# Kernel tuning notes

Hardware: AMD Instinct MI355X
Metric: run time of the kernel (lower is better)

The kernel has to match this reference:

```python
import jax, jax.numpy as jnp
import numpy as np

IN_FEATURES = 8192
OUT_FEATURES = 8192
LOG2_IN = 13
LOG2_OUT = 13
Q_LEVELS = 2 ** 4 - 1  # 15, 4-bit quantization levels


def _rot_mats(angles):
    # (m,) angles -> (m, 2, 2) Givens rotation matrices (QuIP gen_rand_orthos p=2 fast path)
    c, s = jnp.cos(angles), jnp.sin(angles)
    return jnp.stack([jnp.stack([c, s], axis=-1), jnp.stack([-s, c], axis=-1)], axis=-2)


def _mul_ortho_butterfly(angles, p_in, p_out, x):
    # QuIP mul_ortho_butterfly for n = 2^L: input permutation, L stages of
    # block-diagonal 2x2 rotations each followed by a stride-interleave, output permutation.
    n, q = x.shape
    x = x[p_in]
    for i in range(angles.shape[0]):  # static stage count (log2 n)
        B = _rot_mats(angles[i])                             # (n/2, 2, 2)
        x = jnp.einsum('mij,mjq->miq', B, x.reshape(n // 2, 2, q))
        x = jnp.transpose(x, (1, 0, 2)).reshape(n, q)        # interleave stride permutation
    return x[p_out]


def setup_inputs() -> dict:
    key = jax.random.key(0)
    ks = jax.random.split(key, 12)
    x = jax.random.normal(ks[0], (1, IN_FEATURES), dtype=jnp.float32)
    qweight = jax.random.randint(ks[1], (IN_FEATURES, OUT_FEATURES), 0, 16, dtype=jnp.int32)
    # +0.5 keeps the per-feature divisor away from zero (it divides x)
    scaleWH = jax.random.uniform(ks[2], (IN_FEATURES,), dtype=jnp.float32) + 0.5
    scale = jax.random.uniform(ks[3], (), dtype=jnp.float32) + 0.5
    bias = jax.random.normal(ks[4], (OUT_FEATURES,), dtype=jnp.float32)
    two_pi = 2.0 * np.float32(np.pi)
    U_angles = jax.random.uniform(ks[5], (LOG2_OUT, OUT_FEATURES // 2), dtype=jnp.float32) * two_pi
    V_angles = jax.random.uniform(ks[6], (LOG2_IN, IN_FEATURES // 2), dtype=jnp.float32) * two_pi
    pU_in = jax.random.permutation(ks[7], OUT_FEATURES).astype(jnp.int32)
    pU_out = jax.random.permutation(ks[8], OUT_FEATURES).astype(jnp.int32)
    pV_in = jax.random.permutation(ks[9], IN_FEATURES).astype(jnp.int32)
    pV_out = jax.random.permutation(ks[10], IN_FEATURES).astype(jnp.int32)
    return {"x": x, "qweight": qweight, "scaleWH": scaleWH, "scale": scale, "bias": bias,
            "U_angles": U_angles, "V_angles": V_angles,
            "pU_in": pU_in, "pU_out": pU_out, "pV_in": pV_in, "pV_out": pV_out}


def reference(x, qweight, scaleWH, scale, bias, U_angles, V_angles, pU_in, pU_out, pV_in, pV_out):
    # dequantize: w in [0, 15] -> [-1, 1], then global scale
    w = qweight.T.astype(jnp.float32)                 # (out, in)
    w_fast = (w / Q_LEVELS * 2.0 - 1.0) * scale
    h = (x / scaleWH).T                               # (in, 1) reverse diag scaling
    h = _mul_ortho_butterfly(V_angles, pV_in, pV_out, h)   # V^T-side incoherence transform
    h = w_fast @ h                                    # (out, 1) single-token GEMV
    h = _mul_ortho_butterfly(U_angles, pU_in, pU_out, h).T  # (1, out) U-side transform
    return h + bias
```

## Files before the change

### kernel.cpp

```cpp
#include <hip/hip_runtime.h>

#define IN_F   8192
#define OUT_F  8192
#define HALF_F 4096
#define STAGES 13

#define KCHUNK 64
#define NCHUNK (IN_F / KCHUNK)
#define OTILE  1024

typedef int   v4i __attribute__((ext_vector_type(4)));
typedef float v4f __attribute__((ext_vector_type(4)));

__global__ __launch_bounds__(1024) void butterfly_in_kernel(
    const float* __restrict__ x, const float* __restrict__ scaleWH,
    const float* __restrict__ V_angles, const int* __restrict__ pin,
    const int* __restrict__ pout, float* __restrict__ h_out,
    float* __restrict__ sum_out)
{
    __shared__ float bufA[IN_F];
    __shared__ float bufB[IN_F];
    const int tid = threadIdx.x;

#pragma unroll
    for (int j = 0; j < 8; ++j) {
        int k = tid + j * 1024;
        int src = pin[k];
        bufA[k] = x[src] / scaleWH[src];
    }
    __syncthreads();

    float* in = bufA;
    float* out = bufB;
    for (int s = 0; s < STAGES; ++s) {
        const float* ang = V_angles + s * HALF_F;
#pragma unroll
        for (int j = 0; j < 4; ++j) {
            int m = tid + j * 1024;
            float c, sn;
            __sincosf(ang[m], &sn, &c);
            float x0 = in[2 * m];
            float x1 = in[2 * m + 1];
            out[m]          =  c * x0 + sn * x1;
            out[HALF_F + m] = -sn * x0 + c * x1;
        }
        __syncthreads();
        float* t = in; in = out; out = t;
    }

    float local = 0.0f;
#pragma unroll
    for (int j = 0; j < 8; ++j) {
        int k = tid + j * 1024;
        float v = in[pout[k]];
        h_out[k] = v;
        local += v;
    }
    __syncthreads();
    float* red = out;
    red[tid] = local;
    __syncthreads();
    for (int s = 512; s > 0; s >>= 1) {
        if (tid < s) red[tid] += red[tid + s];
        __syncthreads();
    }
    if (tid == 0) *sum_out = red[0];
}

__global__ __launch_bounds__(256) void gemv_kernel(
    const int* __restrict__ q, const float* __restrict__ h,
    float* __restrict__ partials)
{
    __shared__ float hs[KCHUNK];
    const int tid = threadIdx.x;
    const int ot = blockIdx.x;
    const int kc = blockIdx.y;
    const int i0 = kc * KCHUNK;

    if (tid < KCHUNK) hs[tid] = h[i0 + tid];
    __syncthreads();

    const int o = ot * OTILE + tid * 4;
    const int* qp = q + (size_t)i0 * OUT_F + o;

    float a0 = 0.f, a1 = 0.f, a2 = 0.f, a3 = 0.f;
#pragma unroll 4
    for (int ii = 0; ii < KCHUNK; ++ii) {
        v4i v = __builtin_nontemporal_load((const v4i*)qp);
        qp += OUT_F;
        float hv = hs[ii];
        a0 += hv * (float)v[0];
        a1 += hv * (float)v[1];
        a2 += hv * (float)v[2];
        a3 += hv * (float)v[3];
    }
    v4f r; r[0] = a0; r[1] = a1; r[2] = a2; r[3] = a3;
    *(v4f*)(partials + (size_t)kc * OUT_F + o) = r;
}

__global__ __launch_bounds__(256) void reduce_kernel(
    const float* __restrict__ partials, float* __restrict__ accum)
{
    const int o = blockIdx.x * 256 + threadIdx.x;
    float s = 0.0f;
#pragma unroll 8
    for (int c = 0; c < NCHUNK; ++c) s += partials[(size_t)c * OUT_F + o];
    accum[o] = s;
}

__global__ __launch_bounds__(1024) void butterfly_out_kernel(
    const float* __restrict__ accum, const float* __restrict__ sum_h_p,
    const float* __restrict__ scale_p, const float* __restrict__ bias,
    const float* __restrict__ U_angles, const int* __restrict__ pin,
    const int* __restrict__ pout, float* __restrict__ out_f)
{
    __shared__ float bufA[OUT_F];
    __shared__ float bufB[OUT_F];
    const int tid = threadIdx.x;
    const float scale = *scale_p;
    const float sum_h = *sum_h_p;

#pragma unroll
    for (int j = 0; j < 8; ++j) {
        int k = tid + j * 1024;
        bufA[k] = scale * ((2.0f / 15.0f) * accum[k] - sum_h);
    }
    __syncthreads();
#pragma unroll
    for (int j = 0; j < 8; ++j) {
        int k = tid + j * 1024;
        bufB[k] = bufA[pin[k]];
    }
    __syncthreads();

    float* in = bufB;
    float* out = bufA;
    for (int s = 0; s < STAGES; ++s) {
        const float* ang = U_angles + s * HALF_F;
#pragma unroll
        for (int j = 0; j < 4; ++j) {
            int m = tid + j * 1024;
            float c, sn;
            __sincosf(ang[m], &sn, &c);
            float x0 = in[2 * m];
            float x1 = in[2 * m + 1];
            out[m]          =  c * x0 + sn * x1;
            out[HALF_F + m] = -sn * x0 + c * x1;
        }
        __syncthreads();
        float* t = in; in = out; out = t;
    }

#pragma unroll
    for (int j = 0; j < 8; ++j) {
        int k = tid + j * 1024;
        out_f[k] = in[pout[k]] + bias[k];
    }
}

extern "C" void kernel_launch(void* const* d_in, const int* in_sizes, int n_in,
                              void* d_out, int out_size, void* d_ws, size_t ws_size,
                              hipStream_t stream) {
    const float* x        = (const float*)d_in[0];
    const int*   qweight  = (const int*)  d_in[1];
    const float* scaleWH  = (const float*)d_in[2];
    const float* scale    = (const float*)d_in[3];
    const float* bias     = (const float*)d_in[4];
    const float* U_angles = (const float*)d_in[5];
    const float* V_angles = (const float*)d_in[6];
    const int*   pU_in    = (const int*)  d_in[7];
    const int*   pU_out   = (const int*)  d_in[8];
    const int*   pV_in    = (const int*)  d_in[9];
    const int*   pV_out   = (const int*)  d_in[10];
    float* out = (float*)d_out;

    float* h        = (float*)d_ws;
    float* sum_h    = h + IN_F;
    float* accum    = sum_h + 8;
    float* partials = accum + OUT_F;

    butterfly_in_kernel<<<1, 1024, 0, stream>>>(
        x, scaleWH, V_angles, pV_in, pV_out, h, sum_h);

    gemv_kernel<<<dim3(OUT_F / OTILE, NCHUNK), 256, 0, stream>>>(
        qweight, h, partials);

    reduce_kernel<<<OUT_F / 256, 256, 0, stream>>>(partials, accum);

    butterfly_out_kernel<<<1, 1024, 0, stream>>>(
        accum, sum_h, scale, bias, U_angles, pU_in, pU_out, out);
}
```

Baseline: 396.2 us.

## Prefetch weight head into cache during input butterfly, fuse dequant into reduce

While the single-block input butterfly runs, 96 extra blocks read the first part of the quantized weight matrix so it is resident in L2/MALL before the GEMV starts, overlapping weight streaming with the serial butterfly. The dequant affine step moves from the output butterfly into the reduce kernel, which removes one shared-memory pass and a sync. KCHUNK doubles, halving the number of partial sums the reduce must read. The prefetch adds extra memory traffic, and the cached data may be evicted or compete with the butterfly block.

```diff
diff --git a/kernel.cpp b/kernel.cpp
--- a/kernel.cpp
+++ b/kernel.cpp
@@ -5,9 +5,12 @@
 #define HALF_F 4096
 #define STAGES 13
 
-#define KCHUNK 64
+#define KCHUNK 128
 #define NCHUNK (IN_F / KCHUNK)
 #define OTILE  1024
+
+#define PF_BLOCKS 96
+#define PF_ITERS  16
 
 typedef int   v4i __attribute__((ext_vector_type(4)));
 typedef float v4f __attribute__((ext_vector_type(4)));
@@ -16,11 +19,26 @@
     const float* __restrict__ x, const float* __restrict__ scaleWH,
     const float* __restrict__ V_angles, const int* __restrict__ pin,
     const int* __restrict__ pout, float* __restrict__ h_out,
-    float* __restrict__ sum_out)
-{
+    float* __restrict__ sum_out, const int* __restrict__ q,
+    int* __restrict__ scratch)
+{
+    const int tid = threadIdx.x;
+
+    if (blockIdx.x != 0) {
+        const int pf = blockIdx.x - 1;
+        const int* base = q + (size_t)pf * (1024 * PF_ITERS * 4);
+        int acc = 0;
+#pragma unroll
+        for (int it = 0; it < PF_ITERS; ++it) {
+            v4i v = *(const v4i*)(base + (it * 1024 + tid) * 4);
+            acc ^= v[0] ^ v[1] ^ v[2] ^ v[3];
+        }
+        if (tid == 0) scratch[pf] = acc;
+        return;
+    }
+
     __shared__ float bufA[IN_F];
     __shared__ float bufB[IN_F];
-    const int tid = threadIdx.x;
 
 #pragma unroll
     for (int j = 0; j < 8; ++j) {
@@ -99,37 +117,29 @@
 }
 
 __global__ __launch_bounds__(256) void reduce_kernel(
-    const float* __restrict__ partials, float* __restrict__ accum)
+    const float* __restrict__ partials, const float* __restrict__ sum_h_p,
+    const float* __restrict__ scale_p, float* __restrict__ t_out)
 {
     const int o = blockIdx.x * 256 + threadIdx.x;
     float s = 0.0f;
 #pragma unroll 8
     for (int c = 0; c < NCHUNK; ++c) s += partials[(size_t)c * OUT_F + o];
-    accum[o] = s;
+    t_out[o] = (*scale_p) * ((2.0f / 15.0f) * s - (*sum_h_p));
 }
 
 __global__ __launch_bounds__(1024) void butterfly_out_kernel(
-    const float* __restrict__ accum, const float* __restrict__ sum_h_p,
-    const float* __restrict__ scale_p, const float* __restrict__ bias,
+    const float* __restrict__ t, const float* __restrict__ bias,
     const float* __restrict__ U_angles, const int* __restrict__ pin,
     const int* __restrict__ pout, float* __restrict__ out_f)
 {
     __shared__ float bufA[OUT_F];
     __shared__ float bufB[OUT_F];
     const int tid = threadIdx.x;
-    const float scale = *scale_p;
-    const float sum_h = *sum_h_p;
-
-#pragma unroll
-    for (int j = 0; j < 8; ++j) {
-        int k = tid + j * 1024;
-        bufA[k] = scale * ((2.0f / 15.0f) * accum[k] - sum_h);
-    }
-    __syncthreads();
-#pragma unroll
-    for (int j = 0; j < 8; ++j) {
-        int k = tid + j * 1024;
-        bufB[k] = bufA[pin[k]];
+
+#pragma unroll
+    for (int j = 0; j < 8; ++j) {
+        int k = tid + j * 1024;
+        bufB[k] = t[pin[k]];
     }
     __syncthreads();
 
@@ -148,7 +158,7 @@
             out[HALF_F + m] = -sn * x0 + c * x1;
         }
         __syncthreads();
-        float* t = in; in = out; out = t;
+        float* tp = in; in = out; out = tp;
     }
 
 #pragma unroll
@@ -176,17 +186,18 @@
 
     float* h        = (float*)d_ws;
     float* sum_h    = h + IN_F;
-    float* accum    = sum_h + 8;
-    float* partials = accum + OUT_F;
-
-    butterfly_in_kernel<<<1, 1024, 0, stream>>>(
-        x, scaleWH, V_angles, pV_in, pV_out, h, sum_h);
+    float* t        = sum_h + 8;
+    float* partials = t + OUT_F;
+    int*   scratch  = (int*)(partials + (size_t)NCHUNK * OUT_F);
+
+    butterfly_in_kernel<<<1 + PF_BLOCKS, 1024, 0, stream>>>(
+        x, scaleWH, V_angles, pV_in, pV_out, h, sum_h, qweight, scratch);
 
     gemv_kernel<<<dim3(OUT_F / OTILE, NCHUNK), 256, 0, stream>>>(
         qweight, h, partials);
 
-    reduce_kernel<<<OUT_F / 256, 256, 0, stream>>>(partials, accum);
+    reduce_kernel<<<OUT_F / 256, 256, 0, stream>>>(partials, sum_h, scale, t);
 
     butterfly_out_kernel<<<1, 1024, 0, stream>>>(
-        accum, sum_h, scale, bias, U_angles, pU_in, pU_out, out);
-}
+        t, bias, U_angles, pU_in, pU_out, out);
+}
```

After: 401.8 us. No clear change (+1.4%).
